# Optimization experiments

Measured on AMD Instinct MI355X. Metric: run time of the kernel, lower is better.

## Reference

```python
import jax, jax.numpy as jnp
import numpy as np

HID = 2048
HEADS = 16
HD = HID // HEADS  # 128
EPS = 1e-6


def setup_inputs() -> dict:
    key = jax.random.key(0)
    ks = jax.random.split(key, 9)
    s = 1.0 / np.sqrt(HID)
    return {
        "hidden_states": jax.random.normal(ks[0], (4, 4096, HID), jnp.float32),
        "q_w": jax.random.normal(ks[1], (HID, HID), jnp.float32) * s,
        "q_b": jnp.zeros((HID,), jnp.float32),
        "k_w": jax.random.normal(ks[2], (HID, HID), jnp.float32) * s,
        "k_b": jnp.zeros((HID,), jnp.float32),
        "v_w": jax.random.normal(ks[3], (HID, HID), jnp.float32) * s,
        "v_b": jnp.zeros((HID,), jnp.float32),
        "o_w": jax.random.normal(ks[4], (HID, HID), jnp.float32) * s,
        "o_b": jnp.zeros((HID,), jnp.float32),
    }


def _heads(x, b, s):
    # [B,S,HID] -> [B,H,S,Dh]
    return x.reshape(b, s, HEADS, HD).transpose(0, 2, 1, 3)


def reference(hidden_states, q_w, q_b, k_w, k_b, v_w, v_b, o_w, o_b):
    b, s, _ = hidden_states.shape
    # torch Linear: y = x @ W.T + b
    q = _heads(hidden_states @ q_w.T + q_b, b, s)
    k = _heads(hidden_states @ k_w.T + k_b, b, s)
    v = _heads(hidden_states @ v_w.T + v_b, b, s)
    # kernel feature map: elu(x) + 1
    qp = jax.nn.elu(q) + 1.0
    kp = jax.nn.elu(k) + 1.0
    # KV outer-product reduction over sequence: [B,H,Dh,Dh]
    kv = jnp.einsum('bhsd,bhse->bhde', kp, v)
    # normalizer z = q' @ sum_s k'  -> [B,H,S,1]
    z = jnp.einsum('bhsd,bhd->bhs', qp, kp.sum(axis=2))[..., None]
    attn = jnp.einsum('bhsd,bhde->bhse', qp, kv) / (z + EPS)
    out = attn.transpose(0, 2, 1, 3).reshape(b, s, HID)
    return out @ o_w.T + o_b
```

## Files before the change

### kernel.cpp

```cpp
#include <hip/hip_runtime.h>
#include <hip/hip_bf16.h>

#define HIDC 2048
#define NHEADS 16
#define HDIM 128
#define NB 4
#define NS 4096
#define NROWS (NB*NS)
#define QSTR 6144
#define EPSV 1e-6f

typedef __attribute__((ext_vector_type(8))) short s16x8;
typedef __attribute__((ext_vector_type(4))) float f32x4;
typedef __attribute__((ext_vector_type(8))) unsigned short u16x8;

static __device__ __forceinline__ unsigned short f2b(float f) {
  unsigned int u = __float_as_uint(f);
  u += 0x7fffu + ((u >> 16) & 1u);
  return (unsigned short)(u >> 16);
}
static __device__ __forceinline__ float b2f(unsigned short h) {
  return __uint_as_float(((unsigned int)h) << 16);
}

static __device__ __forceinline__ void gload_lds16(const unsigned short* g, unsigned short* l) {
  __builtin_amdgcn_global_load_lds(
      (const __attribute__((address_space(1))) void*)g,
      (__attribute__((address_space(3))) void*)l, 16, 0, 0);
}

__global__ __launch_bounds__(256) void convert_all(
    const float* __restrict__ hs, const float* __restrict__ qw,
    const float* __restrict__ kw, const float* __restrict__ vw,
    const float* __restrict__ ow,
    unsigned short* __restrict__ hsb, unsigned short* __restrict__ qwb,
    unsigned short* __restrict__ kwb, unsigned short* __restrict__ vwb,
    unsigned short* __restrict__ owb)
{
  int bid = blockIdx.x;
  const float* src; unsigned short* dst; size_t base;
  if (bid < 16384) { src = hs; dst = hsb; base = (size_t)bid << 11; }
  else {
    int t = bid - 16384; int wsel = t >> 11; int wb = t & 2047;
    src = wsel == 0 ? qw : wsel == 1 ? kw : wsel == 2 ? vw : ow;
    dst = wsel == 0 ? qwb : wsel == 1 ? kwb : wsel == 2 ? vwb : owb;
    base = (size_t)wb << 11;
  }
  size_t i = base + ((size_t)threadIdx.x << 3);
  float4 a = *(const float4*)(src + i);
  float4 b = *(const float4*)(src + i + 4);
  u16x8 o;
  o[0] = f2b(a.x); o[1] = f2b(a.y); o[2] = f2b(a.z); o[3] = f2b(a.w);
  o[4] = f2b(b.x); o[5] = f2b(b.y); o[6] = f2b(b.z); o[7] = f2b(b.w);
  *(u16x8*)(dst + i) = o;
}

template<int QKV, int OUT_BF16>
__global__ __launch_bounds__(256, 2) void gemm256(
    const unsigned short* __restrict__ A,
    const unsigned short* __restrict__ B0,
    const unsigned short* __restrict__ B1,
    const unsigned short* __restrict__ B2,
    const float* __restrict__ bias0,
    const float* __restrict__ bias1,
    const float* __restrict__ bias2,
    void* __restrict__ Cp,
    int ntile, int astr, int ostr)
{
  __shared__ unsigned short lds[36864];
  const int tid = threadIdx.x;
  const int lane = tid & 63, wid = tid >> 6;
  const int wr = wid >> 1, wc = wid & 1;
  const int l15 = lane & 15, l4 = lane >> 4;

  const int cpx = (int)gridDim.x >> 3;
  const int bidx = (int)blockIdx.x;
  const int wg = (bidx & 7) * cpx + (bidx >> 3);
  const int csz = ntile << 2;
  const int chunk = wg / csz;
  const int t = wg % csz;
  const int bm = ((chunk << 2) + (t & 3)) << 8;
  const int bn = (t >> 2) << 7;

  const unsigned short* Bp = B0;
  const float* bias = bias0;
  bool act = false;
  int bnw = bn;
  if (QKV) {
    int seg = bn >> 11;
    Bp = seg == 0 ? B0 : (seg == 1 ? B1 : B2);
    bias = seg == 0 ? bias0 : (seg == 1 ? bias1 : bias2);
    act = seg < 2;
    bnw = bn & 2047;
  }

  const int srow = lane >> 2;
  const int scol = (((lane & 3) ^ ((srow >> 1) & 3)) << 3);
  const unsigned short* Asrc0 = A + (size_t)(bm + ((wid << 2) << 4) + srow) * astr + scol;
  const unsigned short* Asrc1 = Asrc0 + (size_t)16 * astr;
  const unsigned short* Asrc2 = Asrc0 + (size_t)32 * astr;
  const unsigned short* Asrc3 = Asrc0 + (size_t)48 * astr;
  const unsigned short* Bsrc0 = Bp + (size_t)(bnw + ((wid << 1) << 4) + srow) * HIDC + scol;
  const unsigned short* Bsrc1 = Bsrc0 + (size_t)16 * HIDC;
  const int adst = wid << 11;
  const int bdst = 8192 + (wid << 10);

  const int xa = ((l4 ^ ((l15 >> 1) & 3)) << 3);
  const int abase = ((wr << 7) + l15) * 32 + xa;
  const int bbase = 8192 + ((wc << 6) + l15) * 32 + xa;

  f32x4 acc[8][4] = {};
  s16x8 af[8], bfr[4];

#define STAGE6(sb_, kt_) { \
    gload_lds16(Asrc0 + (kt_), &lds[(sb_) + adst]); \
    gload_lds16(Asrc1 + (kt_), &lds[(sb_) + adst + 512]); \
    gload_lds16(Asrc2 + (kt_), &lds[(sb_) + adst + 1024]); \
    gload_lds16(Asrc3 + (kt_), &lds[(sb_) + adst + 1536]); \
    gload_lds16(Bsrc0 + (kt_), &lds[(sb_) + bdst]); \
    gload_lds16(Bsrc1 + (kt_), &lds[(sb_) + bdst + 512]); }

#define MMROW(mf_) { \
    acc[mf_][0] = __builtin_amdgcn_mfma_f32_16x16x32_bf16(af[mf_], bfr[0], acc[mf_][0], 0, 0, 0); \
    acc[mf_][1] = __builtin_amdgcn_mfma_f32_16x16x32_bf16(af[mf_], bfr[1], acc[mf_][1], 0, 0, 0); \
    acc[mf_][2] = __builtin_amdgcn_mfma_f32_16x16x32_bf16(af[mf_], bfr[2], acc[mf_][2], 0, 0, 0); \
    acc[mf_][3] = __builtin_amdgcn_mfma_f32_16x16x32_bf16(af[mf_], bfr[3], acc[mf_][3], 0, 0, 0); }

#define DO_STEP(GATE, STG, KT) { \
    if ((GATE) == 6)      { asm volatile("s_waitcnt vmcnt(6)" ::: "memory"); } \
    else if ((GATE) == 0) { asm volatile("s_waitcnt vmcnt(0)" ::: "memory"); } \
    __builtin_amdgcn_s_barrier(); \
    bfr[0] = *(const s16x8*)&lds[rb + bbase]; \
    bfr[1] = *(const s16x8*)&lds[rb + bbase + 512]; \
    bfr[2] = *(const s16x8*)&lds[rb + bbase + 1024]; \
    bfr[3] = *(const s16x8*)&lds[rb + bbase + 1536]; \
    af[0] = *(const s16x8*)&lds[rb + abase]; \
    af[1] = *(const s16x8*)&lds[rb + abase + 512]; \
    af[2] = *(const s16x8*)&lds[rb + abase + 1024]; \
    af[3] = *(const s16x8*)&lds[rb + abase + 1536]; \
    af[4] = *(const s16x8*)&lds[rb + abase + 2048]; \
    af[5] = *(const s16x8*)&lds[rb + abase + 2560]; \
    af[6] = *(const s16x8*)&lds[rb + abase + 3072]; \
    af[7] = *(const s16x8*)&lds[rb + abase + 3584]; \
    if (STG) STAGE6(sb, KT); \
    __builtin_amdgcn_sched_barrier(0); \
    __builtin_amdgcn_s_setprio(1); \
    MMROW(0) MMROW(1) MMROW(2) MMROW(3) \
    MMROW(4) MMROW(5) MMROW(6) MMROW(7) \
    __builtin_amdgcn_s_setprio(0); \
    { int t_ = rb; rb = (rb == 24576) ? 0 : rb + 12288; sb = t_; } \
  }

  STAGE6(0, 0);
  STAGE6(12288, 32);
  int rb = 0, sb = 24576;

  for (int s = 0; s < 62; ++s) {
    DO_STEP(6, 1, (s + 2) << 5)
  }
  DO_STEP(0, 0, 0)
  DO_STEP(-1, 0, 0)

#undef DO_STEP
#undef MMROW
#undef STAGE6

  #pragma unroll
  for (int nf = 0; nf < 4; ++nf) {
    const int colw = (wc << 6) + (nf << 4) + l15;
    const float bv = bias[bnw + colw];
    #pragma unroll
    for (int mf = 0; mf < 8; ++mf) {
      #pragma unroll
      for (int r = 0; r < 4; ++r) {
        const int row = bm + (wr << 7) + (mf << 4) + (l4 << 2) + r;
        float v = acc[mf][nf][r] + bv;
        if (QKV) { if (act) v = (v > 0.f) ? (v + 1.f) : __expf(v); }
        const size_t off = (size_t)row * ostr + bn + colw;
        if (OUT_BF16) ((unsigned short*)Cp)[off] = f2b(v);
        else          ((float*)Cp)[off] = v;
      }
    }
  }
}

__global__ __launch_bounds__(256) void kv_partial(
    const unsigned short* __restrict__ kp, const unsigned short* __restrict__ vv,
    float* __restrict__ kvp, float* __restrict__ ksp)
{
  const int bh = blockIdx.x >> 4;
  const int chunk = blockIdx.x & 15;
  const int b = bh >> 4, h = bh & 15;
  const int tid = threadIdx.x;
  const int td = tid >> 4, te = tid & 15;

  __shared__ float kpl[32][128];
  __shared__ float vl[32][132];

  float acc[8][8] = {};
  float ks[8] = {};

  const size_t rowbase = (size_t)b * NS * QSTR + (size_t)h * HDIM;
  const int s0 = chunk * 256;

  for (int st = 0; st < 256; st += 32) {
    __syncthreads();
    #pragma unroll
    for (int i = 0; i < 2; ++i) {
      int idx = tid + (i << 8);
      int row = idx >> 4, q = idx & 15;
      size_t g = rowbase + (size_t)(s0 + st + row) * QSTR + (q << 3);
      u16x8 k8 = *(const u16x8*)(kp + g);
      u16x8 v8 = *(const u16x8*)(vv + g);
      float tk[8], tv[8];
      #pragma unroll
      for (int j = 0; j < 8; ++j) { tk[j] = b2f(k8[j]); tv[j] = b2f(v8[j]); }
      *(float4*)&kpl[row][(q << 3)]     = make_float4(tk[0], tk[1], tk[2], tk[3]);
      *(float4*)&kpl[row][(q << 3) + 4] = make_float4(tk[4], tk[5], tk[6], tk[7]);
      *(float4*)&vl[row][(q << 3)]      = make_float4(tv[0], tv[1], tv[2], tv[3]);
      *(float4*)&vl[row][(q << 3) + 4]  = make_float4(tv[4], tv[5], tv[6], tv[7]);
    }
    __syncthreads();
    #pragma unroll 4
    for (int s = 0; s < 32; ++s) {
      float kd[8], ve[8];
      *(float4*)&kd[0] = *(const float4*)&kpl[s][td << 3];
      *(float4*)&kd[4] = *(const float4*)&kpl[s][(td << 3) + 4];
      *(float4*)&ve[0] = *(const float4*)&vl[s][te << 3];
      *(float4*)&ve[4] = *(const float4*)&vl[s][(te << 3) + 4];
      if (te == 0) {
        #pragma unroll
        for (int i = 0; i < 8; ++i) ks[i] += kd[i];
      }
      #pragma unroll
      for (int i = 0; i < 8; ++i)
        #pragma unroll
        for (int j = 0; j < 8; ++j)
          acc[i][j] += kd[i] * ve[j];
    }
  }

  float* outp = kvp + ((size_t)(chunk * 64 + bh) << 14);
  #pragma unroll
  for (int j = 0; j < 8; ++j) {
    int e = (te << 3) + j;
    float r0[8];
    #pragma unroll
    for (int i = 0; i < 8; ++i) r0[i] = acc[i][j];
    *(float4*)&outp[(size_t)e * HDIM + (td << 3)]     = *(float4*)&r0[0];
    *(float4*)&outp[(size_t)e * HDIM + (td << 3) + 4] = *(float4*)&r0[4];
  }
  if (te == 0) {
    float* kso = ksp + ((size_t)(chunk * 64 + bh) << 7) + (td << 3);
    #pragma unroll
    for (int i = 0; i < 8; ++i) kso[i] = ks[i];
  }
}

__global__ __launch_bounds__(256) void kv_reduce(
    const float* __restrict__ kvp, float* __restrict__ kvT)
{
  int i = blockIdx.x * 256 + threadIdx.x;
  float s = 0.f;
  #pragma unroll
  for (int c = 0; c < 16; ++c) s += kvp[(size_t)c * (64 * 16384) + i];
  kvT[i] = s;
}

__global__ __launch_bounds__(256) void attn_ker(
    const unsigned short* __restrict__ qp, const float* __restrict__ kvT,
    const float* __restrict__ ksp, unsigned short* __restrict__ attn)
{
  const int bh = blockIdx.x >> 5, stile = blockIdx.x & 31;
  const int b = bh >> 4, h = bh & 15;
  const int tid = threadIdx.x;
  const int lane = tid & 63, w = tid >> 6;
  const int l15 = lane & 15, l4 = lane >> 4;

  __shared__ unsigned short Qs[128][136];
  __shared__ unsigned short Ks[128][136];
  __shared__ float ksl[128];
  __shared__ float zs[128];

  const size_t qbase = ((size_t)b * NS + (size_t)stile * 128) * QSTR + (size_t)h * HDIM;

  #pragma unroll
  for (int i = 0; i < 8; ++i) {
    int idx = tid + (i << 8);
    int row = idx >> 4, q = idx & 15;
    u16x8 v8 = *(const u16x8*)(qp + qbase + (size_t)row * QSTR + (q << 3));
    *(u16x8*)&Qs[row][q << 3] = v8;
  }
  const float* kvb = kvT + ((size_t)bh << 14);
  #pragma unroll
  for (int i = 0; i < 16; ++i) {
    int idx = tid + (i << 8);
    int row = idx >> 5, q = idx & 31;
    float4 v4 = *(const float4*)(kvb + (size_t)row * HDIM + (q << 2));
    ushort4 w4; w4.x = f2b(v4.x); w4.y = f2b(v4.y); w4.z = f2b(v4.z); w4.w = f2b(v4.w);
    *(ushort4*)&Ks[row][q << 2] = w4;
  }
  if (tid < 128) {
    float s = 0.f;
    #pragma unroll
    for (int c = 0; c < 16; ++c) s += ksp[((size_t)(c * 64 + bh) << 7) + tid];
    ksl[tid] = s;
  }
  __syncthreads();
  if (tid < 128) {
    float z = 0.f;
    #pragma unroll
    for (int dq = 0; dq < 16; ++dq) {
      u16x8 qv = *(const u16x8*)&Qs[tid][dq << 3];
      #pragma unroll
      for (int j = 0; j < 8; ++j) z += b2f(qv[j]) * ksl[(dq << 3) + j];
    }
    zs[tid] = 1.f / (z + EPSV);
  }
  __syncthreads();

  f32x4 acc[2][8] = {};
  #pragma unroll
  for (int kk = 0; kk < 4; ++kk) {
    s16x8 a[2], bb[8];
    #pragma unroll
    for (int mf = 0; mf < 2; ++mf)
      a[mf] = *(const s16x8*)&Qs[(w << 5) + (mf << 4) + l15][(kk << 5) + (l4 << 3)];
    #pragma unroll
    for (int nf = 0; nf < 8; ++nf)
      bb[nf] = *(const s16x8*)&Ks[(nf << 4) + l15][(kk << 5) + (l4 << 3)];
    #pragma unroll
    for (int mf = 0; mf < 2; ++mf)
      #pragma unroll
      for (int nf = 0; nf < 8; ++nf)
        acc[mf][nf] = __builtin_amdgcn_mfma_f32_16x16x32_bf16(a[mf], bb[nf], acc[mf][nf], 0, 0, 0);
  }

  #pragma unroll
  for (int mf = 0; mf < 2; ++mf) {
    #pragma unroll
    for (int r = 0; r < 4; ++r) {
      const int rl = (w << 5) + (mf << 4) + (l4 << 2) + r;
      const float zi = zs[rl];
      #pragma unroll
      for (int nf = 0; nf < 8; ++nf) {
        const int e = (nf << 4) + l15;
        attn[qbase + (size_t)rl * QSTR + e] = f2b(acc[mf][nf][r] * zi);
      }
    }
  }
}

extern "C" void kernel_launch(void* const* d_in, const int* in_sizes, int n_in,
                              void* d_out, int out_size, void* d_ws, size_t ws_size,
                              hipStream_t stream) {
  const float* hs = (const float*)d_in[0];
  const float* qw = (const float*)d_in[1];
  const float* qb = (const float*)d_in[2];
  const float* kw = (const float*)d_in[3];
  const float* kb = (const float*)d_in[4];
  const float* vw = (const float*)d_in[5];
  const float* vb = (const float*)d_in[6];
  const float* ow = (const float*)d_in[7];
  const float* ob = (const float*)d_in[8];

  char* w = (char*)d_ws;
  unsigned short* hsb = (unsigned short*)(w);
  unsigned short* qwb = (unsigned short*)(w + 67108864);
  unsigned short* kwb = (unsigned short*)(w + 75497472);
  unsigned short* vwb = (unsigned short*)(w + 83886080);
  unsigned short* owb = (unsigned short*)(w + 92274688);
  unsigned short* qkv = (unsigned short*)(w + 100663296);
  float* kvp = (float*)(w);
  float* ksp = (float*)(w + 67108864);
  float* kvT = (float*)(w + 67108864 + 524288);

  convert_all<<<dim3(24576), dim3(256), 0, stream>>>(hs, qw, kw, vw, ow, hsb, qwb, kwb, vwb, owb);
  gemm256<1, 1><<<dim3(3072), dim3(256), 0, stream>>>(
      hsb, qwb, kwb, vwb, qb, kb, vb, qkv, 48, HIDC, QSTR);
  kv_partial<<<dim3(1024), dim3(256), 0, stream>>>(qkv + 2048, qkv + 4096, kvp, ksp);
  kv_reduce<<<dim3(4096), dim3(256), 0, stream>>>(kvp, kvT);
  attn_ker<<<dim3(2048), dim3(256), 0, stream>>>(qkv, kvT, ksp, qkv + 4096);
  gemm256<0, 0><<<dim3(1024), dim3(256), 0, stream>>>(
      qkv + 4096, owb, owb, owb, ob, ob, ob, d_out, 16, QSTR, HIDC);
}
```

Before: 805.5 us.

## Enlarge GEMM tile to 256x256 with 8 waves and 64-deep K double buffering

Both GEMM launches now use 512-thread blocks, each computing a 256x256 output tile instead of 256x128. The tile is split across 8 waves in a 2x4 grid. The K loop now stages 64-wide slabs with two buffers, where before it used three 32-wide buffers, and splits each slab into four MFMA phases with barriers and interleaved global-to-LDS loads. This aims to raise arithmetic intensity and cut global reloads of A and B, at the cost of one block per CU, 128KB of LDS and more barriers per iteration.

```diff
diff --git a/kernel.cpp b/kernel.cpp
--- a/kernel.cpp
+++ b/kernel.cpp
@@ -56,7 +56,7 @@
 }
 
 template<int QKV, int OUT_BF16>
-__global__ __launch_bounds__(256, 2) void gemm256(
+__global__ __launch_bounds__(512, 1) void gemm256(
     const unsigned short* __restrict__ A,
     const unsigned short* __restrict__ B0,
     const unsigned short* __restrict__ B1,
@@ -67,10 +67,10 @@
     void* __restrict__ Cp,
     int ntile, int astr, int ostr)
 {
-  __shared__ unsigned short lds[36864];
+  __shared__ unsigned short lds[65536];
   const int tid = threadIdx.x;
   const int lane = tid & 63, wid = tid >> 6;
-  const int wr = wid >> 1, wc = wid & 1;
+  const int wr = wid >> 2, wc = wid & 3;
   const int l15 = lane & 15, l4 = lane >> 4;
 
   const int cpx = (int)gridDim.x >> 3;
@@ -78,9 +78,9 @@
   const int wg = (bidx & 7) * cpx + (bidx >> 3);
   const int csz = ntile << 2;
   const int chunk = wg / csz;
-  const int t = wg % csz;
-  const int bm = ((chunk << 2) + (t & 3)) << 8;
-  const int bn = (t >> 2) << 7;
+  const int tt = wg % csz;
+  const int bm = ((chunk << 2) + (tt & 3)) << 8;
+  const int bn = (tt >> 2) << 8;
 
   const unsigned short* Bp = B0;
   const float* bias = bias0;
@@ -94,76 +94,104 @@
     bnw = bn & 2047;
   }
 
-  const int srow = lane >> 2;
-  const int scol = (((lane & 3) ^ ((srow >> 1) & 3)) << 3);
-  const unsigned short* Asrc0 = A + (size_t)(bm + ((wid << 2) << 4) + srow) * astr + scol;
-  const unsigned short* Asrc1 = Asrc0 + (size_t)16 * astr;
-  const unsigned short* Asrc2 = Asrc0 + (size_t)32 * astr;
-  const unsigned short* Asrc3 = Asrc0 + (size_t)48 * astr;
-  const unsigned short* Bsrc0 = Bp + (size_t)(bnw + ((wid << 1) << 4) + srow) * HIDC + scol;
-  const unsigned short* Bsrc1 = Bsrc0 + (size_t)16 * HIDC;
-  const int adst = wid << 11;
-  const int bdst = 8192 + (wid << 10);
+  const int r0 = tid >> 2;
+  const int s0 = tid & 3;
+  const int scol = ((s0 ^ ((r0 >> 1) & 3)) << 3);
+  const unsigned short* ApA  = A  + (size_t)(bm  + r0) * astr + scol;
+  const unsigned short* ApA2 = ApA + (size_t)128 * astr;
+  const unsigned short* BpB  = Bp + (size_t)(bnw + r0) * HIDC + scol;
+  const unsigned short* BpB2 = BpB + (size_t)128 * HIDC;
 
   const int xa = ((l4 ^ ((l15 >> 1) & 3)) << 3);
   const int abase = ((wr << 7) + l15) * 32 + xa;
-  const int bbase = 8192 + ((wc << 6) + l15) * 32 + xa;
+  const int bbase = 16384 + ((wc << 6) + l15) * 32 + xa;
 
   f32x4 acc[8][4] = {};
-  s16x8 af[8], bfr[4];
-
-#define STAGE6(sb_, kt_) { \
-    gload_lds16(Asrc0 + (kt_), &lds[(sb_) + adst]); \
-    gload_lds16(Asrc1 + (kt_), &lds[(sb_) + adst + 512]); \
-    gload_lds16(Asrc2 + (kt_), &lds[(sb_) + adst + 1024]); \
-    gload_lds16(Asrc3 + (kt_), &lds[(sb_) + adst + 1536]); \
-    gload_lds16(Bsrc0 + (kt_), &lds[(sb_) + bdst]); \
-    gload_lds16(Bsrc1 + (kt_), &lds[(sb_) + bdst + 512]); }
-
-#define MMROW(mf_) { \
-    acc[mf_][0] = __builtin_amdgcn_mfma_f32_16x16x32_bf16(af[mf_], bfr[0], acc[mf_][0], 0, 0, 0); \
-    acc[mf_][1] = __builtin_amdgcn_mfma_f32_16x16x32_bf16(af[mf_], bfr[1], acc[mf_][1], 0, 0, 0); \
-    acc[mf_][2] = __builtin_amdgcn_mfma_f32_16x16x32_bf16(af[mf_], bfr[2], acc[mf_][2], 0, 0, 0); \
-    acc[mf_][3] = __builtin_amdgcn_mfma_f32_16x16x32_bf16(af[mf_], bfr[3], acc[mf_][3], 0, 0, 0); }
-
-#define DO_STEP(GATE, STG, KT) { \
-    if ((GATE) == 6)      { asm volatile("s_waitcnt vmcnt(6)" ::: "memory"); } \
-    else if ((GATE) == 0) { asm volatile("s_waitcnt vmcnt(0)" ::: "memory"); } \
-    __builtin_amdgcn_s_barrier(); \
-    bfr[0] = *(const s16x8*)&lds[rb + bbase]; \
-    bfr[1] = *(const s16x8*)&lds[rb + bbase + 512]; \
-    bfr[2] = *(const s16x8*)&lds[rb + bbase + 1024]; \
-    bfr[3] = *(const s16x8*)&lds[rb + bbase + 1536]; \
-    af[0] = *(const s16x8*)&lds[rb + abase]; \
-    af[1] = *(const s16x8*)&lds[rb + abase + 512]; \
-    af[2] = *(const s16x8*)&lds[rb + abase + 1024]; \
-    af[3] = *(const s16x8*)&lds[rb + abase + 1536]; \
-    af[4] = *(const s16x8*)&lds[rb + abase + 2048]; \
-    af[5] = *(const s16x8*)&lds[rb + abase + 2560]; \
-    af[6] = *(const s16x8*)&lds[rb + abase + 3072]; \
-    af[7] = *(const s16x8*)&lds[rb + abase + 3584]; \
-    if (STG) STAGE6(sb, KT); \
-    __builtin_amdgcn_sched_barrier(0); \
-    __builtin_amdgcn_s_setprio(1); \
-    MMROW(0) MMROW(1) MMROW(2) MMROW(3) \
-    MMROW(4) MMROW(5) MMROW(6) MMROW(7) \
-    __builtin_amdgcn_s_setprio(0); \
-    { int t_ = rb; rb = (rb == 24576) ? 0 : rb + 12288; sb = t_; } \
-  }
-
-  STAGE6(0, 0);
-  STAGE6(12288, 32);
-  int rb = 0, sb = 24576;
-
-  for (int s = 0; s < 62; ++s) {
-    DO_STEP(6, 1, (s + 2) << 5)
-  }
-  DO_STEP(0, 0, 0)
-  DO_STEP(-1, 0, 0)
-
-#undef DO_STEP
-#undef MMROW
-#undef STAGE6
+  s16x8 af[8], bf2[4];
+
+#define LD(off_) (*(const s16x8*)&lds[off_])
+#define ST_A(kk_, kt_) { \
+    gload_lds16(ApA  + (kt_) + ((kk_) << 5), &lds[wb + ((kk_) << 13) + (tid << 3)]); \
+    gload_lds16(ApA2 + (kt_) + ((kk_) << 5), &lds[wb + ((kk_) << 13) + 4096 + (tid << 3)]); }
+#define ST_B(kk_, kt_) { \
+    gload_lds16(BpB  + (kt_) + ((kk_) << 5), &lds[wb + 16384 + ((kk_) << 13) + (tid << 3)]); \
+    gload_lds16(BpB2 + (kt_) + ((kk_) << 5), &lds[wb + 16384 + ((kk_) << 13) + 4096 + (tid << 3)]); }
+#define MM16(i0_, i1_, i2_, i3_) { \
+    acc[i0_][0] = __builtin_amdgcn_mfma_f32_16x16x32_bf16(af[i0_], bf2[0], acc[i0_][0], 0, 0, 0); \
+    acc[i0_][1] = __builtin_amdgcn_mfma_f32_16x16x32_bf16(af[i0_], bf2[1], acc[i0_][1], 0, 0, 0); \
+    acc[i0_][2] = __builtin_amdgcn_mfma_f32_16x16x32_bf16(af[i0_], bf2[2], acc[i0_][2], 0, 0, 0); \
+    acc[i0_][3] = __builtin_amdgcn_mfma_f32_16x16x32_bf16(af[i0_], bf2[3], acc[i0_][3], 0, 0, 0); \
+    acc[i1_][0] = __builtin_amdgcn_mfma_f32_16x16x32_bf16(af[i1_], bf2[0], acc[i1_][0], 0, 0, 0); \
+    acc[i1_][1] = __builtin_amdgcn_mfma_f32_16x16x32_bf16(af[i1_], bf2[1], acc[i1_][1], 0, 0, 0); \
+    acc[i1_][2] = __builtin_amdgcn_mfma_f32_16x16x32_bf16(af[i1_], bf2[2], acc[i1_][2], 0, 0, 0); \
+    acc[i1_][3] = __builtin_amdgcn_mfma_f32_16x16x32_bf16(af[i1_], bf2[3], acc[i1_][3], 0, 0, 0); \
+    acc[i2_][0] = __builtin_amdgcn_mfma_f32_16x16x32_bf16(af[i2_], bf2[0], acc[i2_][0], 0, 0, 0); \
+    acc[i2_][1] = __builtin_amdgcn_mfma_f32_16x16x32_bf16(af[i2_], bf2[1], acc[i2_][1], 0, 0, 0); \
+    acc[i2_][2] = __builtin_amdgcn_mfma_f32_16x16x32_bf16(af[i2_], bf2[2], acc[i2_][2], 0, 0, 0); \
+    acc[i2_][3] = __builtin_amdgcn_mfma_f32_16x16x32_bf16(af[i2_], bf2[3], acc[i2_][3], 0, 0, 0); \
+    acc[i3_][0] = __builtin_amdgcn_mfma_f32_16x16x32_bf16(af[i3_], bf2[0], acc[i3_][0], 0, 0, 0); \
+    acc[i3_][1] = __builtin_amdgcn_mfma_f32_16x16x32_bf16(af[i3_], bf2[1], acc[i3_][1], 0, 0, 0); \
+    acc[i3_][2] = __builtin_amdgcn_mfma_f32_16x16x32_bf16(af[i3_], bf2[2], acc[i3_][2], 0, 0, 0); \
+    acc[i3_][3] = __builtin_amdgcn_mfma_f32_16x16x32_bf16(af[i3_], bf2[3], acc[i3_][3], 0, 0, 0); }
+#define SB   __builtin_amdgcn_sched_barrier(0);
+#define BAR  __builtin_amdgcn_s_barrier();
+#define LGKM0 asm volatile("s_waitcnt lgkmcnt(0)" ::: "memory");
+#define PRON __builtin_amdgcn_s_setprio(1);
+#define PROFF __builtin_amdgcn_s_setprio(0);
+#define GATE(G_) { if ((G_) == 4) { asm volatile("s_waitcnt vmcnt(4)" ::: "memory"); } \
+                   else if ((G_) == 0) { asm volatile("s_waitcnt vmcnt(0)" ::: "memory"); } }
+
+#define DO_TILE(t_, STG, G1, G3) { \
+    const int rb = ((t_) & 1) << 15; \
+    const int wb = rb ^ 32768; (void)wb; \
+    const int kts = ((t_) + 1) << 6; (void)kts; \
+     \
+    bf2[0] = LD(rb + bbase);        bf2[1] = LD(rb + bbase + 512); \
+    bf2[2] = LD(rb + bbase + 1024); bf2[3] = LD(rb + bbase + 1536); \
+    af[0] = LD(rb + abase);         af[1] = LD(rb + abase + 512); \
+    af[2] = LD(rb + abase + 1024);  af[3] = LD(rb + abase + 1536); \
+    if (STG) ST_A(0, kts); \
+    SB BAR LGKM0 PRON MM16(0, 1, 2, 3) PROFF BAR \
+     \
+    af[4] = LD(rb + abase + 2048);  af[5] = LD(rb + abase + 2560); \
+    af[6] = LD(rb + abase + 3072);  af[7] = LD(rb + abase + 3584); \
+    if (STG) ST_B(0, kts); \
+    SB BAR LGKM0 PRON MM16(4, 5, 6, 7) PROFF GATE(G1) BAR \
+     \
+    bf2[0] = LD(rb + 8192 + bbase);        bf2[1] = LD(rb + 8192 + bbase + 512); \
+    bf2[2] = LD(rb + 8192 + bbase + 1024); bf2[3] = LD(rb + 8192 + bbase + 1536); \
+    af[0] = LD(rb + 8192 + abase);         af[1] = LD(rb + 8192 + abase + 512); \
+    af[2] = LD(rb + 8192 + abase + 1024);  af[3] = LD(rb + 8192 + abase + 1536); \
+    if (STG) ST_A(1, kts); \
+    SB BAR LGKM0 PRON MM16(0, 1, 2, 3) PROFF BAR \
+     \
+    af[4] = LD(rb + 8192 + abase + 2048);  af[5] = LD(rb + 8192 + abase + 2560); \
+    af[6] = LD(rb + 8192 + abase + 3072);  af[7] = LD(rb + 8192 + abase + 3584); \
+    if (STG) ST_B(1, kts); \
+    SB BAR LGKM0 PRON MM16(4, 5, 6, 7) PROFF GATE(G3) BAR \
+  }
+
+  {
+    const int wb = 0;
+    ST_A(0, 0); ST_B(0, 0); ST_A(1, 0); ST_B(1, 0);
+  }
+  asm volatile("s_waitcnt vmcnt(4)" ::: "memory");
+  __builtin_amdgcn_s_barrier();
+
+  for (int t = 0; t < 31; ++t) DO_TILE(t, 1, 4, 4)
+  DO_TILE(31, 0, 0, -1)
+
+#undef DO_TILE
+#undef GATE
+#undef PROFF
+#undef PRON
+#undef LGKM0
+#undef BAR
+#undef SB
+#undef MM16
+#undef ST_B
+#undef ST_A
+#undef LD
 
   #pragma unroll
   for (int nf = 0; nf < 4; ++nf) {
@@ -376,11 +404,11 @@
   float* kvT = (float*)(w + 67108864 + 524288);
 
   convert_all<<<dim3(24576), dim3(256), 0, stream>>>(hs, qw, kw, vw, ow, hsb, qwb, kwb, vwb, owb);
-  gemm256<1, 1><<<dim3(3072), dim3(256), 0, stream>>>(
-      hsb, qwb, kwb, vwb, qb, kb, vb, qkv, 48, HIDC, QSTR);
+  gemm256<1, 1><<<dim3(1536), dim3(512), 0, stream>>>(
+      hsb, qwb, kwb, vwb, qb, kb, vb, qkv, 24, HIDC, QSTR);
   kv_partial<<<dim3(1024), dim3(256), 0, stream>>>(qkv + 2048, qkv + 4096, kvp, ksp);
   kv_reduce<<<dim3(4096), dim3(256), 0, stream>>>(kvp, kvT);
   attn_ker<<<dim3(2048), dim3(256), 0, stream>>>(qkv, kvT, ksp, qkv + 4096);
-  gemm256<0, 0><<<dim3(1024), dim3(256), 0, stream>>>(
-      qkv + 4096, owb, owb, owb, ob, ob, ob, d_out, 16, QSTR, HIDC);
-}
+  gemm256<0, 0><<<dim3(512), dim3(512), 0, stream>>>(
+      qkv + 4096, owb, owb, owb, ob, ob, ob, d_out, 8, QSTR, HIDC);
+}
```

After: 784.5 us. 1.03x faster.
